# Kernel optimization log

Hardware: AMD Instinct MI355X
Metric: run time of the kernel (lower is better)

The kernel has to match this reference:

```python
import jax, jax.numpy as jnp
import numpy as np
from jax import lax

B, T, D = 4, 2048, 1024
H, DK, DV = 8, 128, 256
K_CONV = 4
EPS_RMS = 1e-5


def _causal_conv_silu(x, w, b):
    # x: (B,T,C), w: (C,1,K) depthwise, b: (C,)
    C = x.shape[-1]
    xc = jnp.transpose(x, (0, 2, 1))  # (B,C,T)
    y = lax.conv_general_dilated(
        xc, w, window_strides=(1,), padding=[(K_CONV - 1, 0)],
        dimension_numbers=('NCH', 'OIH', 'NCH'), feature_group_count=C)
    y = y + b[None, :, None]
    y = jnp.transpose(y, (0, 2, 1))  # (B,T,C)
    return jax.nn.silu(y)


def _l2norm(x, eps=1e-12):
    n = jnp.sqrt(jnp.sum(x * x, axis=-1, keepdims=True))
    return x / jnp.maximum(n, eps)


def setup_inputs() -> dict:
    key = jax.random.key(0)
    ks = jax.random.split(key, 20)
    s = 0.02
    inp = {
        'hidden_states': jax.random.normal(ks[0], (B, T, D), jnp.float32),
        'previous_state': jax.random.normal(ks[1], (B, H, DK, DV), jnp.float32) * 0.1,
        'Wq': jax.random.normal(ks[2], (D, H * DK), jnp.float32) * s,
        'Wk': jax.random.normal(ks[3], (D, H * DK), jnp.float32) * s,
        'Wv': jax.random.normal(ks[4], (D, H * DV), jnp.float32) * s,
        'Wa': jax.random.normal(ks[5], (D, H), jnp.float32) * s,
        'Wb': jax.random.normal(ks[6], (D, H), jnp.float32) * s,
        'Wg': jax.random.normal(ks[7], (D, H * DV), jnp.float32) * s,
        'Wo': jax.random.normal(ks[8], (H * DV, D), jnp.float32) * s,
        'qc_w': jax.random.normal(ks[9], (H * DK, 1, K_CONV), jnp.float32) * 0.25,
        'qc_b': jnp.zeros((H * DK,), jnp.float32),
        'kc_w': jax.random.normal(ks[10], (H * DK, 1, K_CONV), jnp.float32) * 0.25,
        'kc_b': jnp.zeros((H * DK,), jnp.float32),
        'vc_w': jax.random.normal(ks[11], (H * DV, 1, K_CONV), jnp.float32) * 0.25,
        'vc_b': jnp.zeros((H * DV,), jnp.float32),
        'o_norm_w': jnp.ones((DV,), jnp.float32),
    }
    A = jax.random.uniform(ks[12], (H,), jnp.float32, 1e-4, 16.0)
    inp['A_log'] = jnp.log(A)
    # depth_init=True: dt in [1e-4, 1e-3]
    u = jax.random.uniform(ks[13], (H,), jnp.float32)
    dt = jnp.exp(u * (np.log(1e-3) - np.log(1e-4)) + np.log(1e-4))
    inp['dt_bias'] = dt + jnp.log(-jnp.expm1(-dt))
    return inp


def reference(hidden_states, previous_state, Wq, Wk, Wv, Wa, Wb, Wg, Wo,
              qc_w, qc_b, kc_w, kc_b, vc_w, vc_b, o_norm_w, A_log, dt_bias):
    b, t, _ = hidden_states.shape
    # projections + causal depthwise conv + silu
    q = _causal_conv_silu(hidden_states @ Wq, qc_w, qc_b).reshape(b, t, H, DK)
    k = _causal_conv_silu(hidden_states @ Wk, kc_w, kc_b).reshape(b, t, H, DK)
    v = _causal_conv_silu(hidden_states @ Wv, vc_w, vc_b).reshape(b, t, H, DV)
    # gates
    g = -jnp.exp(A_log) * jax.nn.softplus(hidden_states @ Wa + dt_bias)  # (B,T,H)
    alpha = jnp.exp(g)
    beta = jax.nn.sigmoid(hidden_states @ Wb)  # (B,T,H)
    # qk L2 norm
    q = _l2norm(q)
    k = _l2norm(k)

    def step(state, xs):
        q_t, k_t, v_t, a_t, b_t = xs
        o_t = jnp.einsum('bhkv,bhk->bhv', state, q_t)  # read state BEFORE update
        delta = v_t - jnp.einsum('bhkv,bhk->bhv', state, k_t)
        state = a_t[..., None, None] * state + \
            b_t[..., None, None] * jnp.einsum('bhv,bhk->bhkv', delta, k_t)
        return state, o_t

    xs = (jnp.transpose(q, (1, 0, 2, 3)), jnp.transpose(k, (1, 0, 2, 3)),
          jnp.transpose(v, (1, 0, 2, 3)), jnp.transpose(alpha, (1, 0, 2)),
          jnp.transpose(beta, (1, 0, 2)))
    final_state, o = lax.scan(step, previous_state, xs)
    o = jnp.transpose(o, (1, 0, 2, 3))  # (B,T,H,DV)
    # gated RMSNorm per head-v dim
    gate = (hidden_states @ Wg).reshape(b, t, H, DV)
    of = o.astype(jnp.float32)
    var = jnp.mean(of * of, axis=-1, keepdims=True)
    o = (o_norm_w * (of * lax.rsqrt(var + EPS_RMS)).astype(o.dtype)) * jax.nn.sigmoid(gate)
    out = o.reshape(b, t, H * DV) @ Wo  # (B,T,D)
    return out, final_state
```

## Files before the change

### kernel.cpp

```cpp
#include <hip/hip_runtime.h>
#include <stdint.h>

typedef unsigned short u16;
typedef unsigned int u32;

#define DEVFN __device__ __forceinline__

constexpr int CB = 4;
constexpr int CT = 2048;
constexpr int CD = 1024;
constexpr int CH = 8;
constexpr int CDK = 128;
constexpr int CDV = 256;
constexpr long NROW = (long)CB * CT;

DEVFN float b2f(u16 s){ return __uint_as_float(((u32)s) << 16); }
DEVFN u16 f2b(float f){
  u32 u = __float_as_uint(f);
  u32 r = (u + 0x7fffu + ((u >> 16) & 1u)) >> 16;
  return (u16)r;
}
DEVFN float sigm(float x){ return 1.f / (1.f + expf(-x)); }
DEVFN int swz3(int r){ return (r ^ (r >> 2)) & 3; }

__global__ __launch_bounds__(256) void prep_all_k(
    const float* __restrict__ X, u16* __restrict__ Xb,
    const float* __restrict__ Wa, const float* __restrict__ Wb, u16* __restrict__ Wab,
    const float* __restrict__ Wq, const float* __restrict__ Wk, const float* __restrict__ Wv,
    const float* __restrict__ Wg, const float* __restrict__ Wo,
    u16* __restrict__ Wqkvt, u16* __restrict__ Wgt, u16* __restrict__ Wot)
{
  __shared__ float tile[32][33];
  int bid = blockIdx.x;
  if (bid < 2048){
    long i = (long)bid * 256 + threadIdx.x;
    long n4 = NROW * CD / 4;
    long stride = 2048L * 256;
    for (; i < n4; i += stride){
      float4 v = ((const float4*)X)[i];
      ushort4 r;
      r.x = f2b(v.x); r.y = f2b(v.y); r.z = f2b(v.z); r.w = f2b(v.w);
      ((ushort4*)Xb)[i] = r;
    }
    return;
  }
  if (bid < 2112){
    int idx = (bid - 2048) * 256 + threadIdx.x;
    int c = idx >> 10, k = idx & 1023;
    float v = (c < 8) ? Wa[k * 8 + c] : Wb[k * 8 + (c - 8)];
    Wab[c * 1024 + k] = f2b(v);
    return;
  }
  int tb = bid - 2112;
  const float* W; u16* Wt; int K, N, local;
  if (tb < 1024){ W = Wq; Wt = Wqkvt; K = 1024; N = 1024; local = tb; }
  else if (tb < 2048){ W = Wk; Wt = Wqkvt + (size_t)1024 * 1024; K = 1024; N = 1024; local = tb - 1024; }
  else if (tb < 4096){ W = Wv; Wt = Wqkvt + (size_t)2048 * 1024; K = 1024; N = 2048; local = tb - 2048; }
  else if (tb < 6144){ W = Wg; Wt = Wgt; K = 1024; N = 2048; local = tb - 4096; }
  else { W = Wo; Wt = Wot; K = 2048; N = 1024; local = tb - 6144; }
  int sh = (N == 1024) ? 5 : 6;
  int bx = local & ((1 << sh) - 1), by = local >> sh;
  int n0 = bx * 32, k0 = by * 32;

  int tx = threadIdx.x & 31, ty = threadIdx.x >> 5;
  #pragma unroll
  for (int i = 0; i < 4; i++)
    tile[ty + 8*i][tx] = W[(long)(k0 + ty + 8*i) * N + n0 + tx];
  __syncthreads();
  #pragma unroll
  for (int i = 0; i < 4; i++){
    int nn = ty + 8*i;
    Wt[(long)(n0 + nn) * K + k0 + tx] = f2b(tile[tx][nn]);
  }
}

typedef __bf16 bf16x8 __attribute__((ext_vector_type(8)));
typedef float f32x4 __attribute__((ext_vector_type(4)));

DEVFN void store_c(float* p, float v){ *p = v; }
DEVFN void store_c(u16* p, float v){ *p = f2b(v); }

DEVFN void gload16(const void* g, void* l){
  __builtin_amdgcn_global_load_lds((__attribute__((address_space(1))) void*)g,
                                   (__attribute__((address_space(3))) void*)l, 16, 0, 0);
}

template <typename OutT>
__global__ __launch_bounds__(256) void gemm128_k(
    const u16* __restrict__ A, const u16* __restrict__ Bt, OutT* __restrict__ C,
    int M, int N, int K)
{
  __shared__ u16 As[2][128 * 64];
  __shared__ u16 Bs[2][128 * 64];
  int tid = threadIdx.x;
  int lane = tid & 63, wv = tid >> 6;
  int wm = wv & 1, wn = wv >> 1;
  int l15 = lane & 15, lhi = lane >> 4;
  int m0 = blockIdx.y * 128, n0 = blockIdx.x * 128;
  const u16* Ab = A + (long)m0 * K;
  const u16* Bb = Bt + (long)n0 * K;

  auto stage = [&](int t, int bf){
    int k0 = t * 64;
    #pragma unroll
    for (int p = 0; p < 4; p++){
      int X = p * 256 + tid;
      int r = X >> 3, jj = X & 7;
      gload16(Ab + (long)r * K + k0 + ((jj ^ (r & 7)) * 8), &As[bf][(size_t)X * 8]);
    }
    #pragma unroll
    for (int p = 0; p < 4; p++){
      int X = p * 256 + tid;
      int r = X >> 3, jj = X & 7;
      gload16(Bb + (long)r * K + k0 + ((jj ^ (r & 7)) * 8), &Bs[bf][(size_t)X * 8]);
    }
  };

  f32x4 acc[4][4] = {};

  stage(0, 0);
  int T = K >> 6;
  for (int t = 0; t < T; t++){
    int bf = t & 1;
    if (t + 1 < T){
      stage(t + 1, bf ^ 1);
      asm volatile("s_waitcnt vmcnt(8)" ::: "memory");
    } else {
      asm volatile("s_waitcnt vmcnt(0)" ::: "memory");
    }
    __builtin_amdgcn_s_barrier();

    #pragma unroll
    for (int kk = 0; kk < 64; kk += 32){
      int s = (kk >> 3) + lhi;
      bf16x8 av[4], bv[4];
      #pragma unroll
      for (int m = 0; m < 4; m++){
        int r = wm * 64 + m * 16 + l15;
        av[m] = *(const bf16x8*)&As[bf][r * 64 + ((s ^ (r & 7)) * 8)];
      }
      #pragma unroll
      for (int n = 0; n < 4; n++){
        int r = wn * 64 + n * 16 + l15;
        bv[n] = *(const bf16x8*)&Bs[bf][r * 64 + ((s ^ (r & 7)) * 8)];
      }
      #pragma unroll
      for (int m = 0; m < 4; m++)
        #pragma unroll
        for (int n = 0; n < 4; n++)
          acc[m][n] = __builtin_amdgcn_mfma_f32_16x16x32_bf16(av[m], bv[n], acc[m][n], 0, 0, 0);
    }
    asm volatile("" ::: "memory");
    __builtin_amdgcn_s_barrier();
  }

  #pragma unroll
  for (int m = 0; m < 4; m++)
    #pragma unroll
    for (int n = 0; n < 4; n++)
      #pragma unroll
      for (int j = 0; j < 4; j++){
        long row = m0 + wm * 64 + m * 16 + lhi * 4 + j;
        long col = n0 + wn * 64 + n * 16 + l15;
        store_c(&C[row * (long)N + col], acc[m][n][j]);
      }
}

__global__ __launch_bounds__(256) void ab_mfma_k(
    const u16* __restrict__ Xb, const u16* __restrict__ Wab,
    const float* __restrict__ A_log, const float* __restrict__ dt_bias,
    float* __restrict__ alpha, float* __restrict__ beta)
{
  __shared__ u16 Ws[16 * 1024];
  int tid = threadIdx.x, lane = tid & 63, wv = tid >> 6;
  #pragma unroll
  for (int p = 0; p < 8; p++){
    int X = p * 256 + tid;
    int r = X >> 7, s = X & 127;
    gload16(Wab + r * 1024 + (s ^ (r & 7)) * 8, &Ws[(size_t)X * 8]);
  }
  int l15 = lane & 15, lhi = lane >> 4;
  int row0 = blockIdx.x * 64 + wv * 16;
  const u16* Arow = Xb + (long)(row0 + l15) * 1024 + lhi * 8;
  __syncthreads();

  f32x4 acc = {0.f, 0.f, 0.f, 0.f};
  #pragma unroll 8
  for (int ks = 0; ks < 32; ks++){
    bf16x8 av = *(const bf16x8*)(Arow + ks * 32);
    int slot = ks * 4 + lhi;
    bf16x8 bv = *(const bf16x8*)&Ws[l15 * 1024 + (slot ^ (l15 & 7)) * 8];
    acc = __builtin_amdgcn_mfma_f32_16x16x32_bf16(av, bv, acc, 0, 0, 0);
  }

  int col = l15;
  float nA = 0.f, db = 0.f;
  if (col < 8){ nA = -expf(A_log[col]); db = dt_bias[col]; }
  #pragma unroll
  for (int j = 0; j < 4; j++){
    long row = row0 + lhi * 4 + j;
    float v = acc[j];
    if (col < 8){
      float xv = v + db;
      float sp = fmaxf(xv, 0.f) + log1pf(expf(-fabsf(xv)));
      alpha[row * 8 + col] = expf(nA * sp);
    } else {
      beta[row * 8 + (col - 8)] = sigm(v);
    }
  }
}

__global__ __launch_bounds__(64) void conv_all_k(
    const u16* __restrict__ pre,
    const float* __restrict__ qcw, const float* __restrict__ qcb,
    const float* __restrict__ kcw, const float* __restrict__ kcb,
    const float* __restrict__ vcw, const float* __restrict__ vcb,
    u16* __restrict__ qn, u16* __restrict__ kn, u16* __restrict__ vn)
{
  int bid = blockIdx.x;
  int sec = bid & 3;
  int h = (bid >> 2) & 7;
  int tg = (bid >> 5) & 255;
  int b = bid >> 13;
  int t0 = tg * 8;
  int c2 = threadIdx.x * 2;
  const float *cw, *cb; int col; u16* outp; int ostride, ocol; bool norm;
  if (sec == 0){ int ch = h*128 + c2; cw = qcw + ch*4; cb = qcb + ch; col = ch;        outp = qn; ostride = 1024; ocol = ch; norm = true; }
  else if (sec == 1){ int ch = h*128 + c2; cw = kcw + ch*4; cb = kcb + ch; col = 1024+ch; outp = kn; ostride = 1024; ocol = ch; norm = true; }
  else { int z = sec - 2; int ch = h*256 + z*128 + c2; cw = vcw + ch*4; cb = vcb + ch; col = 2048+ch; outp = vn; ostride = 2048; ocol = ch; norm = false; }

  const u16* base = pre + ((long)b * CT) * 4096 + col;
  float wa = cw[0], wb = cw[1], wc = cw[2], wd = cw[3];
  float wa1 = cw[4], wb1 = cw[5], wc1 = cw[6], wd1 = cw[7];
  float bs0 = cb[0], bs1 = cb[1];

  u32 rr[11];
  #pragma unroll
  for (int i = 0; i < 11; i++){
    int t = t0 - 3 + i;
    rr[i] = (t >= 0) ? *(const u32*)(base + (long)t * 4096) : 0u;
  }
  #pragma unroll
  for (int tt = 0; tt < 8; tt++){
    int t = t0 + tt;
    float x0a = b2f((u16)(rr[tt] & 0xffffu)),     x1a = b2f((u16)(rr[tt] >> 16));
    float x0b = b2f((u16)(rr[tt + 1] & 0xffffu)), x1b = b2f((u16)(rr[tt + 1] >> 16));
    float x0c = b2f((u16)(rr[tt + 2] & 0xffffu)), x1c = b2f((u16)(rr[tt + 2] >> 16));
    float x0d = b2f((u16)(rr[tt + 3] & 0xffffu)), x1d = b2f((u16)(rr[tt + 3] >> 16));
    float a0 = fmaf(wa, x0a, fmaf(wb, x0b, fmaf(wc, x0c, fmaf(wd, x0d, bs0))));
    float a1 = fmaf(wa1, x1a, fmaf(wb1, x1b, fmaf(wc1, x1c, fmaf(wd1, x1d, bs1))));
    float y0 = a0 * sigm(a0), y1 = a1 * sigm(a1);
    if (norm){
      float ss = y0 * y0 + y1 * y1;
      #pragma unroll
      for (int off = 1; off < 64; off <<= 1) ss += __shfl_xor(ss, off);
      float inv = 1.f / fmaxf(sqrtf(ss), 1e-12f);
      y0 *= inv; y1 *= inv;
    }
    u32 r = (u32)f2b(y0) | ((u32)f2b(y1) << 16);
    *(u32*)(outp + ((long)b * CT + t) * ostride + ocol) = r;
  }
}

__global__ __launch_bounds__(256) void chunk_meta_k(
    const u16* __restrict__ qn, const u16* __restrict__ kn, const u16* __restrict__ vn,
    const float* __restrict__ alpha, const float* __restrict__ beta,
    u16* __restrict__ TGK_g, u16* __restrict__ TVT_g, u16* __restrict__ P_g,
    u16* __restrict__ KTS_g, float* __restrict__ scal_g)
{
  int bid = blockIdx.x;
  int c = bid & 63, bh = bid >> 6;
  int b = bh >> 3, h = bh & 7;
  long rowb = (long)b * CT + c * 32;
  int tid = threadIdx.x, lane = tid & 63, wv = tid >> 6;
  int l15 = lane & 15, lhi = lane >> 4;
  int mt = wv & 1, nt = wv >> 1;

  __shared__ u16 Kc[4096], Qc[4096], Vl[8192];
  __shared__ u16 Vt[10240];
  __shared__ u16 KTG[5120];
  __shared__ u16 TinvL[1280];
  __shared__ float Al[32 * 33];
  __shared__ float al_s[32], be_s[32], cums[33], bscal[32], gsl[32];

  #pragma unroll
  for (int p = 0; p < 2; p++){
    int X = p * 256 + tid; int r = X >> 4, jj = X & 15;
    gload16(kn + ((rowb + r) * 8 + h) * 128 + (jj ^ (r & 7)) * 8, &Kc[(size_t)X * 8]);
  }
  #pragma unroll
  for (int p = 0; p < 2; p++){
    int X = p * 256 + tid; int r = X >> 4, jj = X & 15;
    gload16(qn + ((rowb + r) * 8 + h) * 128 + (jj ^ (r & 7)) * 8, &Qc[(size_t)X * 8]);
  }
  #pragma unroll
  for (int p = 0; p < 4; p++){
    int X = p * 256 + tid; int r = X >> 5, cc = X & 31;
    gload16(vn + ((rowb + r) * 8 + h) * 256 + cc * 8, &Vl[(size_t)X * 8]);
  }
  if (tid < 32) al_s[tid] = alpha[(rowb + tid) * 8 + h];
  else if (tid < 64) be_s[tid - 32] = beta[(rowb + tid - 32) * 8 + h];
  __syncthreads();
  if (tid == 0){
    float cacc = 0.f; cums[0] = 0.f;
    for (int j = 0; j < 32; j++){ cacc += logf(al_s[j]); cums[j + 1] = cacc; }
  }
  __syncthreads();
  if (tid < 32){
    bscal[tid] = be_s[tid] * expf(cums[32] - cums[tid + 1]);
    gsl[tid] = expf(cums[tid]);
  }
  asm volatile("s_waitcnt vmcnt(0)" ::: "memory");
  __syncthreads();

  #pragma unroll
  for (int i = 0; i < 16; i++){
    u32 lo = Vl[(2 * i) * 256 + tid];
    u32 hi = Vl[(2 * i + 1) * 256 + tid];
    *(u32*)&Vt[tid * 40 + 2 * i] = lo | (hi << 16);
  }

  f32x4 rk = {0.f,0.f,0.f,0.f}, rq = {0.f,0.f,0.f,0.f};
  int ra = mt * 16 + l15, rb = nt * 16 + l15;
  #pragma unroll
  for (int ks = 0; ks < 4; ks++){
    int slot = ks * 4 + lhi;
    bf16x8 ak = *(const bf16x8*)&Kc[ra * 128 + (slot ^ (ra & 7)) * 8];
    bf16x8 aq = *(const bf16x8*)&Qc[ra * 128 + (slot ^ (ra & 7)) * 8];
    bf16x8 bk = *(const bf16x8*)&Kc[rb * 128 + (slot ^ (rb & 7)) * 8];
    rk = __builtin_amdgcn_mfma_f32_16x16x32_bf16(ak, bk, rk, 0, 0, 0);
    rq = __builtin_amdgcn_mfma_f32_16x16x32_bf16(aq, bk, rq, 0, 0, 0);
  }
  int s_ = nt * 16 + l15;
  long pb_ = (long)bid * 1024;
  #pragma unroll
  for (int j = 0; j < 4; j++){
    int i_ = mt * 16 + lhi * 4 + j;
    float e = (s_ < i_) ? expf(cums[i_] - cums[s_ + 1]) * be_s[s_] : 0.f;
    Al[i_ * 33 + s_] = rk[j] * e;
    P_g[pb_ + i_ * 32 + s_] = f2b(rq[j] * e);
  }
  __syncthreads();

  if (tid < 32){
    float x[32];
    #pragma unroll
    for (int i = 0; i < 32; i++) x[i] = (i == tid) ? 1.f : 0.f;
    #pragma unroll
    for (int s = 0; s < 31; s++){
      float xs = x[s];
      #pragma unroll
      for (int i = s + 1; i < 32; i++) x[i] = fmaf(-Al[i * 33 + s], xs, x[i]);
    }
    #pragma unroll
    for (int i = 0; i < 32; i++) TinvL[i * 40 + tid] = f2b(x[i]);
    scal_g[(long)bid * 48 + tid] = gsl[tid];
    if (tid == 0) scal_g[(long)bid * 48 + 32] = expf(cums[32]);
  } else if (tid >= 64){
    int t0 = tid - 64;
    #pragma unroll
    for (int e2 = 0; e2 < 22; e2++){
      int e = t0 + e2 * 192;
      if (e < 4096){
        int k = e >> 5, s2 = e & 31;
        int slot = k >> 3;
        float kv = b2f(Kc[s2 * 128 + (slot ^ (s2 & 7)) * 8 + (k & 7)]);
        KTS_g[(long)bid * 4096 + k * 32 + s2] = f2b(kv * bscal[s2]);
        KTG[k * 40 + s2] = f2b(kv * gsl[s2]);
      }
    }
  }
  __syncthreads();

  long tb = (long)bid * 4096;
  #pragma unroll
  for (int p = 0; p < 4; p++){
    int idx = wv * 4 + p; int ts = idx >> 3, tk = idx & 7;
    bf16x8 aT = *(const bf16x8*)&TinvL[(ts * 16 + l15) * 40 + lhi * 8];
    bf16x8 bK2 = *(const bf16x8*)&KTG[(tk * 16 + l15) * 40 + lhi * 8];
    f32x4 z = {0.f,0.f,0.f,0.f};
    f32x4 d = __builtin_amdgcn_mfma_f32_16x16x32_bf16(aT, bK2, z, 0, 0, 0);
    #pragma unroll
    for (int j = 0; j < 4; j++)
      TGK_g[tb + (ts * 16 + lhi * 4 + j) * 128 + tk * 16 + l15] = f2b(d[j]);
  }
  long vb = (long)bid * 8192;
  #pragma unroll
  for (int p = 0; p < 8; p++){
    int idx = wv * 8 + p; int tv = idx >> 1, ts2 = idx & 1;
    bf16x8 aV = *(const bf16x8*)&Vt[(tv * 16 + l15) * 40 + lhi * 8];
    bf16x8 bT2 = *(const bf16x8*)&TinvL[(ts2 * 16 + l15) * 40 + lhi * 8];
    f32x4 z = {0.f,0.f,0.f,0.f};
    f32x4 d = __builtin_amdgcn_mfma_f32_16x16x32_bf16(aV, bT2, z, 0, 0, 0);
    #pragma unroll
    for (int j = 0; j < 4; j++)
      TVT_g[vb + (tv * 16 + lhi * 4 + j) * 32 + ts2 * 16 + l15] = f2b(d[j]);
  }
}

__global__ __launch_bounds__(256) void chunk_scan_k(
    const u16* __restrict__ qn, const u16* __restrict__ TGK_g, const u16* __restrict__ TVT_g,
    const u16* __restrict__ P_g, const u16* __restrict__ KTS_g,
    const float* __restrict__ scal_g, const float* __restrict__ prev,
    u16* __restrict__ obuf, float* __restrict__ fstate)
{
  int bid = blockIdx.x;
  int bh = bid & 31, vs = bid >> 5;
  int b = bh >> 3, h = bh & 7;
  int tid = threadIdx.x, lane = tid & 63, wv = tid >> 6;
  int l15 = lane & 15, lhi = lane >> 4;
  int mv = wv & 1, nn = wv >> 1;

  __shared__ u16 TG[2][4096];
  __shared__ u16 Qc[2][4096];
  __shared__ u16 TVs[2][1024];
  __shared__ float scal[2][48];
  __shared__ u16 KT[2][4096];
  __shared__ u16 Ps[2][1024];
  __shared__ u16 Sb[32 * 136];
  __shared__ u16 Ub[32 * 40];

  auto issue_g1 = [&](int c, int bf){
    long cb_ = (long)bh * 64 + c;
    const u16* Tb_ = TGK_g + cb_ * 4096;
    #pragma unroll
    for (int p = 0; p < 2; p++){
      int X = p * 256 + tid; int r = X >> 4, jj = X & 15;
      gload16(Tb_ + r * 128 + (jj ^ (r & 7)) * 8, &TG[bf][(size_t)X * 8]);
    }
    long rowb = (long)b * CT + c * 32;
    #pragma unroll
    for (int p = 0; p < 2; p++){
      int X = p * 256 + tid; int r = X >> 4, jj = X & 15;
      gload16(qn + ((rowb + r) * 8 + h) * 128 + (jj ^ (r & 7)) * 8, &Qc[bf][(size_t)X * 8]);
    }
    if (lane < 32){
      int X = wv * 32 + lane; int r = X >> 2, jj = X & 3;
      gload16(TVT_g + cb_ * 8192 + (vs * 32 + r) * 32 + (jj ^ swz3(r)) * 8, &TVs[bf][(size_t)X * 8]);
    }
    long sbase = cb_ * 48;
    #pragma unroll
    for (int p = 0; p < 3; p++){
      int X = wv * 3 + p;
      if (lane == 0) gload16(scal_g + sbase + X * 4, &scal[bf][X * 4]);
    }
  };
  auto issue_g2 = [&](int c, int bf){
    long cb_ = (long)bh * 64 + c;
    const u16* Kb_ = KTS_g + cb_ * 4096;
    #pragma unroll
    for (int p = 0; p < 2; p++){
      int X = p * 256 + tid; int r = X >> 2, jj = X & 3;
      gload16(Kb_ + (r * 4 + (jj ^ swz3(r))) * 8, &KT[bf][(size_t)X * 8]);
    }
    if (lane < 32){
      int X = wv * 32 + lane; int r = X >> 2, jj = X & 3;
      gload16(P_g + cb_ * 1024 + (r * 4 + (jj ^ swz3(r))) * 8, &Ps[bf][(size_t)X * 8]);
    }
  };

  issue_g1(0, 0);
  issue_g2(0, 0);
  f32x4 st[4];
  {
    const float* pbv = prev + ((long)bh * 128) * 256 + vs * 32;
    #pragma unroll
    for (int tt = 0; tt < 4; tt++){
      int k = (nn * 4 + tt) * 16 + l15;
      #pragma unroll
      for (int j = 0; j < 4; j++){
        int v = mv * 16 + lhi * 4 + j;
        st[tt][j] = pbv[(long)k * 256 + v];
      }
    }
  }
  #pragma unroll
  for (int tt = 0; tt < 4; tt++){
    int k = (nn * 4 + tt) * 16 + l15;
    #pragma unroll
    for (int j = 0; j < 4; j++){
      int v = mv * 16 + lhi * 4 + j;
      Sb[v * 136 + k] = f2b(st[tt][j]);
    }
  }
  asm volatile("s_waitcnt vmcnt(3) lgkmcnt(0)" ::: "memory");
  __builtin_amdgcn_s_barrier();

  int rv = mv * 16 + l15, ri = nn * 16 + l15;
  for (int c = 0; c < 64; ++c){
    int bf = c & 1;
    f32x4 us = {0.f,0.f,0.f,0.f}, o1 = {0.f,0.f,0.f,0.f};
    #pragma unroll
    for (int ks = 0; ks < 4; ks++){
      bf16x8 aS = *(const bf16x8*)&Sb[rv * 136 + ks * 32 + lhi * 8];
      int slot = ks * 4 + lhi;
      bf16x8 bT = *(const bf16x8*)&TG[bf][ri * 128 + (slot ^ (ri & 7)) * 8];
      bf16x8 bQ = *(const bf16x8*)&Qc[bf][ri * 128 + (slot ^ (ri & 7)) * 8];
      us = __builtin_amdgcn_mfma_f32_16x16x32_bf16(aS, bT, us, 0, 0, 0);
      o1 = __builtin_amdgcn_mfma_f32_16x16x32_bf16(aS, bQ, o1, 0, 0, 0);
    }
    if (c + 1 < 64) issue_g1(c + 1, bf ^ 1);
    #pragma unroll
    for (int j = 0; j < 4; j++){
      int v = mv * 16 + lhi * 4 + j;
      float tv = b2f(TVs[bf][v * 32 + ((ri >> 3) ^ swz3(v)) * 8 + (ri & 7)]);
      Ub[v * 40 + ri] = f2b(tv - us[j]);
    }
    asm volatile("s_waitcnt lgkmcnt(0)" ::: "memory");
    if (c + 1 < 64) asm volatile("s_waitcnt vmcnt(8)" ::: "memory");
    else            asm volatile("s_waitcnt vmcnt(0)" ::: "memory");
    __builtin_amdgcn_s_barrier();

    float Gt = scal[bf][32];
    f32x4 oacc;
    {
      bf16x8 aU = *(const bf16x8*)&Ub[rv * 40 + lhi * 8];
      bf16x8 bP = *(const bf16x8*)&Ps[bf][ri * 32 + (lhi ^ swz3(ri)) * 8];
      f32x4 z = {0.f,0.f,0.f,0.f};
      oacc = __builtin_amdgcn_mfma_f32_16x16x32_bf16(aU, bP, z, 0, 0, 0);
      #pragma unroll
      for (int tt = 0; tt < 4; tt++){
        int rk_ = (nn * 4 + tt) * 16 + l15;
        bf16x8 bK = *(const bf16x8*)&KT[bf][rk_ * 32 + (lhi ^ swz3(rk_)) * 8];
        f32x4 ci = st[tt] * Gt;
        st[tt] = __builtin_amdgcn_mfma_f32_16x16x32_bf16(aU, bK, ci, 0, 0, 0);
      }
    }
    {
      float gi = scal[bf][ri];
      ushort4 pk;
      pk.x = f2b(oacc[0] + gi * o1[0]);
      pk.y = f2b(oacc[1] + gi * o1[1]);
      pk.z = f2b(oacc[2] + gi * o1[2]);
      pk.w = f2b(oacc[3] + gi * o1[3]);
      *(ushort4*)&obuf[(((long)bh * CT) + c * 32 + ri) * 256 + vs * 32 + mv * 16 + lhi * 4] = pk;
    }
    if (c + 1 < 64) issue_g2(c + 1, bf ^ 1);
    #pragma unroll
    for (int tt = 0; tt < 4; tt++){
      int k = (nn * 4 + tt) * 16 + l15;
      #pragma unroll
      for (int j = 0; j < 4; j++){
        int v = mv * 16 + lhi * 4 + j;
        Sb[v * 136 + k] = f2b(st[tt][j]);
      }
    }
    asm volatile("s_waitcnt lgkmcnt(0)" ::: "memory");
    if (c + 1 < 64) asm volatile("s_waitcnt vmcnt(3)" ::: "memory");
    else            asm volatile("s_waitcnt vmcnt(0)" ::: "memory");
    __builtin_amdgcn_s_barrier();
  }

  {
    float* fb = fstate + ((long)bh * 128) * 256 + vs * 32;
    #pragma unroll
    for (int tt = 0; tt < 4; tt++){
      int k = (nn * 4 + tt) * 16 + l15;
      #pragma unroll
      for (int j = 0; j < 4; j++){
        int v = mv * 16 + lhi * 4 + j;
        fb[(long)k * 256 + v] = st[tt][j];
      }
    }
  }
}

__global__ __launch_bounds__(256) void rms_gate_k(
    const u16* __restrict__ o, const u16* __restrict__ gate,
    const float* __restrict__ nw, u16* __restrict__ ofin)
{
  long idx = (long)blockIdx.x * 4 + (threadIdx.x >> 6);
  int lane = threadIdx.x & 63;
  int h = (int)(idx & 7);
  long bt = idx >> 3;
  int b = (int)(bt >> 11);
  long t = bt & (CT - 1);
  long obase = (((long)(b * 8 + h)) * CT + t) * CDV + lane * 4;
  long base = idx * CDV + lane * 4;
  ushort4 o4 = *(const ushort4*)(o + obase);
  float ox = b2f(o4.x), oy = b2f(o4.y), oz = b2f(o4.z), ow = b2f(o4.w);
  float ss = ox*ox + oy*oy + oz*oz + ow*ow;
  #pragma unroll
  for (int off = 1; off < 64; off <<= 1) ss += __shfl_xor(ss, off);
  float r = rsqrtf(ss * (1.f / CDV) + 1e-5f);
  ushort4 g4 = *(const ushort4*)(gate + base);
  float w0 = nw[lane*4], w1 = nw[lane*4+1], w2 = nw[lane*4+2], w3 = nw[lane*4+3];
  ushort4 res;
  res.x = f2b(ox * r * w0 * sigm(b2f(g4.x)));
  res.y = f2b(oy * r * w1 * sigm(b2f(g4.y)));
  res.z = f2b(oz * r * w2 * sigm(b2f(g4.z)));
  res.w = f2b(ow * r * w3 * sigm(b2f(g4.w)));
  *(ushort4*)(ofin + base) = res;
}

extern "C" void kernel_launch(void* const* d_in, const int* in_sizes, int n_in,
                              void* d_out, int out_size, void* d_ws, size_t ws_size,
                              hipStream_t stream)
{
  (void)in_sizes; (void)n_in; (void)out_size; (void)ws_size;
  const float* X    = (const float*)d_in[0];
  const float* prev = (const float*)d_in[1];
  const float* Wq   = (const float*)d_in[2];
  const float* Wk   = (const float*)d_in[3];
  const float* Wv   = (const float*)d_in[4];
  const float* Wa   = (const float*)d_in[5];
  const float* Wb   = (const float*)d_in[6];
  const float* Wg   = (const float*)d_in[7];
  const float* Wo   = (const float*)d_in[8];
  const float* qcw  = (const float*)d_in[9];
  const float* qcb  = (const float*)d_in[10];
  const float* kcw  = (const float*)d_in[11];
  const float* kcb  = (const float*)d_in[12];
  const float* vcw  = (const float*)d_in[13];
  const float* vcb  = (const float*)d_in[14];
  const float* onw  = (const float*)d_in[15];
  const float* Alog = (const float*)d_in[16];
  const float* dtb  = (const float*)d_in[17];

  float* out = (float*)d_out;
  float* fstate = out + (long)CB * CT * CD;

  char* ws = (char*)d_ws;
  size_t off = 0;
  auto alloc = [&](size_t bytes) -> char* {
    char* p = ws + off;
    off += (bytes + 255) & ~(size_t)255;
    return p;
  };
  u16* Xb     = (u16*)alloc(NROW * CD * 2);
  u16* Wqkvt  = (u16*)alloc((size_t)4096 * 1024 * 2);
  u16* Wgt    = (u16*)alloc((size_t)2048 * 1024 * 2);
  u16* Wot    = (u16*)alloc((size_t)1024 * 2048 * 2);
  u16* qkvpre = (u16*)alloc(NROW * 4096 * 2);
  u16* gpre   = (u16*)alloc(NROW * 2048 * 2);
  float* alpha = (float*)alloc(NROW * 8 * 4);
  float* beta  = (float*)alloc(NROW * 8 * 4);
  u16* qn   = (u16*)alloc(NROW * 1024 * 2);
  u16* kn   = (u16*)alloc(NROW * 1024 * 2);
  u16* vn   = (u16*)alloc(NROW * 2048 * 2);
  u16* ofin = (u16*)alloc(NROW * 2048 * 2);
  u16* Wab  = (u16*)alloc((size_t)16 * 1024 * 2);
  u16* TGK_g  = Xb;
  u16* TVT_g  = ofin;
  u16* obuf   = qkvpre;
  u16* P_g    = qkvpre + (size_t)16777216;
  float* scal_g = (float*)(qkvpre + (size_t)18874368);
  u16* KTS_g  = qkvpre + (size_t)19136512;

  prep_all_k<<<10304, 256, 0, stream>>>(X, Xb, Wa, Wb, Wab,
                                        Wq, Wk, Wv, Wg, Wo, Wqkvt, Wgt, Wot);

  gemm128_k<u16><<<dim3(32, 64), 256, 0, stream>>>(Xb, Wqkvt, qkvpre, 8192, 4096, 1024);
  gemm128_k<u16><<<dim3(16, 64), 256, 0, stream>>>(Xb, Wgt, gpre, 8192, 2048, 1024);
  ab_mfma_k<<<128, 256, 0, stream>>>(Xb, Wab, Alog, dtb, alpha, beta);

  conv_all_k<<<CB * (CT / 8) * CH * 4, 64, 0, stream>>>(qkvpre, qcw, qcb, kcw, kcb, vcw, vcb,
                                                        qn, kn, vn);

  chunk_meta_k<<<2048, 256, 0, stream>>>(qn, kn, vn, alpha, beta,
                                         TGK_g, TVT_g, P_g, KTS_g, scal_g);
  chunk_scan_k<<<256, 256, 0, stream>>>(qn, TGK_g, TVT_g, P_g, KTS_g, scal_g,
                                        prev, obuf, fstate);

  rms_gate_k<<<CB * CT * CH / 4, 256, 0, stream>>>(obuf, gpre, onw, ofin);
  gemm128_k<float><<<dim3(8, 64), 256, 0, stream>>>(ofin, Wot, out, 8192, 1024, 2048);
}
```

Baseline: 381.9 us.

## Use 256x256 eight-phase pipelined GEMM for QKV and gate projections

Adds a 512-thread GEMM kernel with 256x256 output tiles whose K loop is split into eight phases. Each phase issues async global-to-LDS loads for a future sub-tile while MFMAs run on the current one, with barriers and s_setprio to interleave waves. The larger tile cuts how often global memory is re-read per output and keeps memory traffic overlapped with compute. The cost is fewer blocks (512 and 256) with one block per CU, heavier register pressure from 32 accumulators per thread, and hand-tuned vmcnt waits that must match the load schedule exactly.

New measurement: 388.7 us. Within noise of the previous version (+1.8%).

```diff
diff --git a/kernel.cpp b/kernel.cpp
--- a/kernel.cpp
+++ b/kernel.cpp
@@ -83,6 +83,115 @@
 DEVFN void gload16(const void* g, void* l){
   __builtin_amdgcn_global_load_lds((__attribute__((address_space(1))) void*)g,
                                    (__attribute__((address_space(3))) void*)l, 16, 0, 0);
+}
+
+DEVFN void do_phase(const u16* __restrict__ Ah, const u16* __restrict__ Bk, int kk,
+                    f32x4* accm, int wm, int wn, int l15, int lhi)
+{
+  bf16x8 av[4], bv[4];
+  #pragma unroll
+  for (int mm = 0; mm < 4; mm++){
+    int lr = wm * 64 + mm * 16 + l15;
+    int s = (kk * 4 + lhi) ^ (lr & 7);
+    av[mm] = *(const bf16x8*)&Ah[lr * 64 + s * 8];
+  }
+  #pragma unroll
+  for (int n = 0; n < 4; n++){
+    int row = wn * 64 + n * 16 + l15;
+    int sb = lhi ^ ((row & 3) ^ ((row >> 2) & 3));
+    bv[n] = *(const bf16x8*)&Bk[row * 32 + sb * 8];
+  }
+  asm volatile("" ::: "memory");
+  __builtin_amdgcn_s_barrier();
+  __builtin_amdgcn_s_setprio(1);
+  #pragma unroll
+  for (int mm = 0; mm < 4; mm++)
+    #pragma unroll
+    for (int n = 0; n < 4; n++)
+      accm[mm * 4 + n] = __builtin_amdgcn_mfma_f32_16x16x32_bf16(av[mm], bv[n], accm[mm * 4 + n], 0, 0, 0);
+  __builtin_amdgcn_s_setprio(0);
+  asm volatile("" ::: "memory");
+  __builtin_amdgcn_s_barrier();
+}
+
+template <typename OutT>
+__global__ __launch_bounds__(512, 1) void gemm256_8ph_k(
+    const u16* __restrict__ A, const u16* __restrict__ Bt, OutT* __restrict__ C,
+    int M, int N, int K)
+{
+  __shared__ u16 Asl[2][2][8192];
+  __shared__ u16 Bsl[2][2][8192];
+  int tid = threadIdx.x;
+  int lane = tid & 63, wv = tid >> 6;
+  int wm = wv & 1, wn = wv >> 1;
+  int l15 = lane & 15, lhi = lane >> 4;
+  int m0 = blockIdx.y * 256, n0 = blockIdx.x * 256;
+  const u16* Ab = A + (long)m0 * K;
+  const u16* Bb = Bt + (long)n0 * K;
+
+  auto stA = [&](int t, int h){
+    u16* dst = &Asl[t & 1][h][0];
+    #pragma unroll
+    for (int p = 0; p < 2; p++){
+      int X = p * 512 + tid;
+      int lr = X >> 3, j = X & 7;
+      int gr = h * 64 + (lr & 63) + ((lr >> 6) << 7);
+      gload16(Ab + (long)gr * K + t * 64 + ((j ^ (lr & 7)) * 8), dst + (size_t)X * 8);
+    }
+  };
+  auto stB = [&](int t, int kh){
+    u16* dst = &Bsl[t & 1][kh][0];
+    #pragma unroll
+    for (int p = 0; p < 2; p++){
+      int X = p * 512 + tid;
+      int row = X >> 2, j = X & 3;
+      int sw = (row & 3) ^ ((row >> 2) & 3);
+      gload16(Bb + (long)row * K + t * 64 + kh * 32 + ((j ^ sw) * 8), dst + (size_t)X * 8);
+    }
+  };
+
+  f32x4 acc[32] = {};
+  int NT = K >> 6, NI = NT >> 1;
+
+  stA(0, 0); stB(0, 0); stA(0, 1); stB(0, 1); stA(1, 0); stB(1, 0);
+  asm volatile("s_waitcnt vmcnt(4)" ::: "memory");
+  __builtin_amdgcn_s_barrier();
+
+  for (int i = 0; i < NI; i++){
+    int e = 2 * i, o = e + 1;
+    bool nl = (i + 1 < NI);
+    stA(o, 1);
+    do_phase(&Asl[0][0][0], &Bsl[0][0][0], 0, &acc[0], wm, wn, l15, lhi);
+    stB(o, 1);
+    do_phase(&Asl[0][0][0], &Bsl[0][1][0], 1, &acc[0], wm, wn, l15, lhi);
+    if (nl) stA(e + 2, 0);
+    do_phase(&Asl[0][1][0], &Bsl[0][0][0], 0, &acc[16], wm, wn, l15, lhi);
+    if (nl) stB(e + 2, 0);
+    if (nl) asm volatile("s_waitcnt vmcnt(4)" ::: "memory");
+    else    asm volatile("s_waitcnt vmcnt(0)" ::: "memory");
+    do_phase(&Asl[0][1][0], &Bsl[0][1][0], 1, &acc[16], wm, wn, l15, lhi);
+    if (nl) stA(e + 2, 1);
+    do_phase(&Asl[1][0][0], &Bsl[1][0][0], 0, &acc[0], wm, wn, l15, lhi);
+    if (nl) stB(e + 2, 1);
+    do_phase(&Asl[1][0][0], &Bsl[1][1][0], 1, &acc[0], wm, wn, l15, lhi);
+    if (nl) stA(o + 2, 0);
+    do_phase(&Asl[1][1][0], &Bsl[1][0][0], 0, &acc[16], wm, wn, l15, lhi);
+    if (nl) stB(o + 2, 0);
+    if (nl) asm volatile("s_waitcnt vmcnt(4)" ::: "memory");
+    else    asm volatile("s_waitcnt vmcnt(0)" ::: "memory");
+    do_phase(&Asl[1][1][0], &Bsl[1][1][0], 1, &acc[16], wm, wn, l15, lhi);
+  }
+
+  #pragma unroll
+  for (int m = 0; m < 8; m++)
+    #pragma unroll
+    for (int n = 0; n < 4; n++)
+      #pragma unroll
+      for (int j = 0; j < 4; j++){
+        long row = m0 + wm * 128 + m * 16 + lhi * 4 + j;
+        long col = n0 + wn * 64 + n * 16 + l15;
+        store_c(&C[row * (long)N + col], acc[m * 4 + n][j]);
+      }
 }
 
 template <typename OutT>
@@ -650,8 +759,8 @@
   prep_all_k<<<10304, 256, 0, stream>>>(X, Xb, Wa, Wb, Wab,
                                         Wq, Wk, Wv, Wg, Wo, Wqkvt, Wgt, Wot);
 
-  gemm128_k<u16><<<dim3(32, 64), 256, 0, stream>>>(Xb, Wqkvt, qkvpre, 8192, 4096, 1024);
-  gemm128_k<u16><<<dim3(16, 64), 256, 0, stream>>>(Xb, Wgt, gpre, 8192, 2048, 1024);
+  gemm256_8ph_k<u16><<<dim3(16, 32), 512, 0, stream>>>(Xb, Wqkvt, qkvpre, 8192, 4096, 1024);
+  gemm256_8ph_k<u16><<<dim3(8, 32), 512, 0, stream>>>(Xb, Wgt, gpre, 8192, 2048, 1024);
   ab_mfma_k<<<128, 256, 0, stream>>>(Xb, Wab, Alog, dtb, alpha, beta);
 
   conv_all_k<<<CB * (CT / 8) * CH * 4, 64, 0, stream>>>(qkvpre, qcw, qcb, kcw, kcb, vcw, vcb,
```
